# Optimization experiments

Measured on AMD Instinct MI355X. Metric: run time of the kernel, lower is better.

Reference implementation:

```python
import jax, jax.numpy as jnp
import numpy as np

N = 100000
E = 600000
D = 128


def setup_inputs() -> dict:
    key = jax.random.key(0)
    k_h, k_src, k_dst, k_W, k_b, k_H = jax.random.split(key, 6)
    h = jax.random.normal(k_h, (N, D), dtype=jnp.float32)
    src = jax.random.randint(k_src, (E,), 0, N, dtype=jnp.int64)
    dst = jax.random.randint(k_dst, (E,), 0, N, dtype=jnp.int64)
    # Linear layer params (PyTorch convention: y = x @ W_w.T + W_b)
    bound_lin = 1.0 / np.sqrt(D)
    W_w = jax.random.uniform(k_W, (D, D), dtype=jnp.float32, minval=-bound_lin, maxval=bound_lin)
    W_b = jax.random.uniform(k_b, (D,), dtype=jnp.float32, minval=-bound_lin, maxval=bound_lin)
    # H = normal(0, 1/D) + I
    H = jax.random.normal(k_H, (D, D), dtype=jnp.float32) * (1.0 / D) + jnp.eye(D, dtype=jnp.float32)
    return {"h": h, "src": src, "dst": dst, "W_w": W_w, "W_b": W_b, "H": H}


def reference(h, src, dst, W_w, W_b, H):
    # node transform: hp = W(h)
    hp = h @ W_w.T + W_b  # [N, D]
    # precompute hp @ H at node level (equivalent to (hp[dst]) @ H, cheaper)
    hpH = hp @ H  # [N, D]
    diff = hp[src] - hpH[dst]  # [E, D] edge-wise gather + sub
    score = jnp.sum(diff * diff, axis=-1)  # [E]
    return score
```

## Files before the change

kernel.cpp:

```cpp
#include <hip/hip_runtime.h>
#include <hip/hip_bf16.h>


#define D 128
#define BN 256
#define BM 64

typedef __attribute__((ext_vector_type(8))) short bf16x8;
typedef __attribute__((ext_vector_type(4))) float f32x4;

static __device__ inline unsigned short f2bf(float x) {
  union { float f; unsigned int u; } v;
  v.f = x;
  unsigned int r = v.u + 0x7fffu + ((v.u >> 16) & 1u);
  return (unsigned short)(r >> 16);
}

__global__ __launch_bounds__(256) void prep_frag_kernel(
    const float* __restrict__ Ww, const float* __restrict__ Wb,
    const float* __restrict__ H, short* __restrict__ Wfrag,
    float* __restrict__ bias_cat) {
  const int b = blockIdx.x;
  const int w = b >> 2;
  const int jt = b & 3;
  const int tid = threadIdx.x;
  const int ks = tid >> 6;
  const int lane = tid & 63;
  const int j = w * 64 + jt * 16 + (lane & 15);
  const int kb = ks * 32 + ((lane >> 4) << 3);

  unsigned short u[8];
  if (w < 2) {
    const float4 lo = *(const float4*)(Ww + j * D + kb);
    const float4 hi = *(const float4*)(Ww + j * D + kb + 4);
    u[0] = f2bf(lo.x); u[1] = f2bf(lo.y); u[2] = f2bf(lo.z); u[3] = f2bf(lo.w);
    u[4] = f2bf(hi.x); u[5] = f2bf(hi.y); u[6] = f2bf(hi.z); u[7] = f2bf(hi.w);
  } else {
    const int jj = j - D;
    float a0 = 0.f, a1 = 0.f, a2 = 0.f, a3 = 0.f;
    float a4 = 0.f, a5 = 0.f, a6 = 0.f, a7 = 0.f;
#pragma unroll 8
    for (int m = 0; m < D; ++m) {
      const float hm = H[m * D + jj];
      const float4 lo = *(const float4*)(Ww + m * D + kb);
      const float4 hi = *(const float4*)(Ww + m * D + kb + 4);
      a0 = fmaf(lo.x, hm, a0); a1 = fmaf(lo.y, hm, a1);
      a2 = fmaf(lo.z, hm, a2); a3 = fmaf(lo.w, hm, a3);
      a4 = fmaf(hi.x, hm, a4); a5 = fmaf(hi.y, hm, a5);
      a6 = fmaf(hi.z, hm, a6); a7 = fmaf(hi.w, hm, a7);
    }
    u[0] = f2bf(a0); u[1] = f2bf(a1); u[2] = f2bf(a2); u[3] = f2bf(a3);
    u[4] = f2bf(a4); u[5] = f2bf(a5); u[6] = f2bf(a6); u[7] = f2bf(a7);
  }
  const int F = ((w * 4 + jt) * 4 + ks) * 64 + lane;
  *(uint4*)(Wfrag + (size_t)F * 8) = *(const uint4*)u;

  if (tid < 16) {
    const int jb = w * 64 + jt * 16 + tid;
    float bv;
    if (w < 2) {
      bv = Wb[jb];
    } else {
      bv = 0.f;
      const int jj = jb - D;
#pragma unroll 8
      for (int m = 0; m < D; ++m) bv = fmaf(Wb[m], H[m * D + jj], bv);
    }
    bias_cat[jb] = bv;
  }
}

__global__ __launch_bounds__(256, 4) void phase1_mfma(
    const float* __restrict__ h, const short* __restrict__ Wfrag,
    const float* __restrict__ bias_cat, short* __restrict__ hp,
    short* __restrict__ hpH, int n_nodes) {
  const int tid = threadIdx.x;
  const int lane = tid & 63;
  const int w = tid >> 6;
  const int base = blockIdx.x * BM;

  f32x4 acc[4][4];
#pragma unroll
  for (int jt = 0; jt < 4; ++jt) {
    const float4 b4 =
        *(const float4*)(bias_cat + w * 64 + jt * 16 + ((lane >> 4) << 2));
    const f32x4 bi = {b4.x, b4.y, b4.z, b4.w};
#pragma unroll
    for (int nt = 0; nt < 4; ++nt) acc[jt][nt] = bi;
  }

  const bf16x8* Wf = (const bf16x8*)Wfrag;
  const int kb = (lane >> 4) << 3;

#pragma unroll
  for (int ks = 0; ks < 4; ++ks) {
    bf16x8 hf[4];
#pragma unroll
    for (int nt = 0; nt < 4; ++nt) {
      int node = base + nt * 16 + (lane & 15);
      if (node >= n_nodes) node = n_nodes - 1;
      const float* hrow = h + (size_t)node * D + ks * 32 + kb;
      const float4 lo = *(const float4*)hrow;
      const float4 hi = *(const float4*)(hrow + 4);
      union { bf16x8 v; unsigned short u[8]; } pk;
      pk.u[0] = f2bf(lo.x); pk.u[1] = f2bf(lo.y);
      pk.u[2] = f2bf(lo.z); pk.u[3] = f2bf(lo.w);
      pk.u[4] = f2bf(hi.x); pk.u[5] = f2bf(hi.y);
      pk.u[6] = f2bf(hi.z); pk.u[7] = f2bf(hi.w);
      hf[nt] = pk.v;
    }
#pragma unroll
    for (int jt = 0; jt < 4; ++jt) {
      const bf16x8 wf = Wf[(((w * 4 + jt) * 4 + ks) << 6) + lane];
#pragma unroll
      for (int nt = 0; nt < 4; ++nt) {
        acc[jt][nt] = __builtin_amdgcn_mfma_f32_16x16x32_bf16(
            wf, hf[nt], acc[jt][nt], 0, 0, 0);
      }
    }
  }

  short* outb = (w < 2) ? hp : hpH;
  const int jb = (w & 1) * 64 + ((lane >> 4) << 2);
#pragma unroll
  for (int jt = 0; jt < 4; ++jt) {
#pragma unroll
    for (int nt = 0; nt < 4; ++nt) {
      const int node = base + nt * 16 + (lane & 15);
      if (node < n_nodes) {
        uint2 pk;
        pk.x = (unsigned int)f2bf(acc[jt][nt][0]) |
               ((unsigned int)f2bf(acc[jt][nt][1]) << 16);
        pk.y = (unsigned int)f2bf(acc[jt][nt][2]) |
               ((unsigned int)f2bf(acc[jt][nt][3]) << 16);
        *(uint2*)(outb + (size_t)node * D + jb + jt * 16) = pk;
      }
    }
  }
}

__global__ __launch_bounds__(256) void edge_kernel(
    const short* __restrict__ hp, const short* __restrict__ hpH,
    const int* __restrict__ src, const int* __restrict__ dst,
    float* __restrict__ score, int n_edges) {
  const int lane = threadIdx.x & 15;
  const int e = (blockIdx.x * 256 + threadIdx.x) >> 4;
  if (e >= n_edges) return;

  const int s = src[e];
  const int d = dst[e];
  const uint4 av = *(const uint4*)(hp + (size_t)s * D + lane * 8);
  const uint4 bv = *(const uint4*)(hpH + (size_t)d * D + lane * 8);

  const unsigned int au[4] = {av.x, av.y, av.z, av.w};
  const unsigned int bu[4] = {bv.x, bv.y, bv.z, bv.w};
  float acc = 0.f;
#pragma unroll
  for (int i = 0; i < 4; ++i) {
    const float alo = __uint_as_float(au[i] << 16);
    const float ahi = __uint_as_float(au[i] & 0xffff0000u);
    const float blo = __uint_as_float(bu[i] << 16);
    const float bhi = __uint_as_float(bu[i] & 0xffff0000u);
    float t = alo - blo;
    acc = fmaf(t, t, acc);
    t = ahi - bhi;
    acc = fmaf(t, t, acc);
  }

  acc += __shfl_xor(acc, 1, 64);
  acc += __shfl_xor(acc, 2, 64);
  acc += __shfl_xor(acc, 4, 64);
  acc += __shfl_xor(acc, 8, 64);

  if (lane == 0) __builtin_nontemporal_store(acc, &score[e]);
}

extern "C" void kernel_launch(void* const* d_in, const int* in_sizes, int n_in,
                              void* d_out, int out_size, void* d_ws,
                              size_t ws_size, hipStream_t stream) {
  const float* h = (const float*)d_in[0];
  const int* src = (const int*)d_in[1];
  const int* dst = (const int*)d_in[2];
  const float* Ww = (const float*)d_in[3];
  const float* Wb = (const float*)d_in[4];
  const float* H = (const float*)d_in[5];
  float* score = (float*)d_out;

  const int n_nodes = in_sizes[0] / D;
  const int n_edges = in_sizes[1];

  char* ws = (char*)d_ws;
  short* hp = (short*)ws;
  short* hpH = hp + (size_t)n_nodes * D;
  short* Wfrag = hpH + (size_t)n_nodes * D;
  float* bias_cat = (float*)(Wfrag + 4096 * 8);

  prep_frag_kernel<<<dim3(16), dim3(256), 0, stream>>>(Ww, Wb, H, Wfrag,
                                                       bias_cat);

  const int nblk = (n_nodes + BM - 1) / BM;
  phase1_mfma<<<dim3(nblk), dim3(256), 0, stream>>>(h, Wfrag, bias_cat, hp,
                                                    hpH, n_nodes);

  const int eblk = (n_edges * 16 + 255) / 256;
  edge_kernel<<<dim3(eblk), dim3(256), 0, stream>>>(hp, hpH, src, dst, score,
                                                    n_edges);
}
```

Before: 188.2 us.

## Stage bf16 node tile in LDS once per block, shared across warps

Previously each of the 4 waves loaded and converted the same 64-node fp32 h tile from global memory, so the block read and converted it four times. Now the block cooperatively loads it once, converts it to bf16 MFMA fragments in shared memory, and every wave reads fragments from LDS after a barrier. The loops are reordered so W fragments are loaded per jt, and the occupancy hint rises from 4 to 6 blocks per CU. This adds 16KB of LDS per block and a sync, which may limit occupancy.

```diff
diff --git a/kernel.cpp b/kernel.cpp
--- a/kernel.cpp
+++ b/kernel.cpp
@@ -70,15 +70,34 @@
   }
 }
 
-__global__ __launch_bounds__(256, 4) void phase1_mfma(
+__global__ __launch_bounds__(256, 6) void phase1_mfma(
     const float* __restrict__ h, const short* __restrict__ Wfrag,
     const float* __restrict__ bias_cat, short* __restrict__ hp,
     short* __restrict__ hpH, int n_nodes) {
+  __shared__ short Hf[1024 * 8];
+
   const int tid = threadIdx.x;
   const int lane = tid & 63;
   const int w = tid >> 6;
   const int base = blockIdx.x * BM;
 
+#pragma unroll
+  for (int i = 0; i < 4; ++i) {
+    const int f = tid + i * 256;
+    const int fl = f & 63;
+    const int nt = (f >> 6) & 3;
+    const int ks = f >> 8;
+    int node = base + nt * 16 + (fl & 15);
+    if (node >= n_nodes) node = n_nodes - 1;
+    const int kb = ks * 32 + ((fl >> 4) << 3);
+    const float4 lo = *(const float4*)(h + (size_t)node * D + kb);
+    const float4 hi = *(const float4*)(h + (size_t)node * D + kb + 4);
+    unsigned short u[8];
+    u[0] = f2bf(lo.x); u[1] = f2bf(lo.y); u[2] = f2bf(lo.z); u[3] = f2bf(lo.w);
+    u[4] = f2bf(hi.x); u[5] = f2bf(hi.y); u[6] = f2bf(hi.z); u[7] = f2bf(hi.w);
+    ((uint4*)Hf)[f] = *(const uint4*)u;
+  }
+
   f32x4 acc[4][4];
 #pragma unroll
   for (int jt = 0; jt < 4; ++jt) {
@@ -89,33 +108,23 @@
     for (int nt = 0; nt < 4; ++nt) acc[jt][nt] = bi;
   }
 
+  __syncthreads();
+
   const bf16x8* Wf = (const bf16x8*)Wfrag;
-  const int kb = (lane >> 4) << 3;
-
-#pragma unroll
-  for (int ks = 0; ks < 4; ++ks) {
-    bf16x8 hf[4];
+  const bf16x8* Hf8 = (const bf16x8*)Hf;
+#pragma unroll
+  for (int jt = 0; jt < 4; ++jt) {
+    bf16x8 wf[4];
+#pragma unroll
+    for (int ks = 0; ks < 4; ++ks)
+      wf[ks] = Wf[(((w * 4 + jt) * 4 + ks) << 6) + lane];
 #pragma unroll
     for (int nt = 0; nt < 4; ++nt) {
-      int node = base + nt * 16 + (lane & 15);
-      if (node >= n_nodes) node = n_nodes - 1;
-      const float* hrow = h + (size_t)node * D + ks * 32 + kb;
-      const float4 lo = *(const float4*)hrow;
-      const float4 hi = *(const float4*)(hrow + 4);
-      union { bf16x8 v; unsigned short u[8]; } pk;
-      pk.u[0] = f2bf(lo.x); pk.u[1] = f2bf(lo.y);
-      pk.u[2] = f2bf(lo.z); pk.u[3] = f2bf(lo.w);
-      pk.u[4] = f2bf(hi.x); pk.u[5] = f2bf(hi.y);
-      pk.u[6] = f2bf(hi.z); pk.u[7] = f2bf(hi.w);
-      hf[nt] = pk.v;
-    }
-#pragma unroll
-    for (int jt = 0; jt < 4; ++jt) {
-      const bf16x8 wf = Wf[(((w * 4 + jt) * 4 + ks) << 6) + lane];
-#pragma unroll
-      for (int nt = 0; nt < 4; ++nt) {
+#pragma unroll
+      for (int ks = 0; ks < 4; ++ks) {
+        const bf16x8 hf = Hf8[((ks << 2) + nt) * 64 + lane];
         acc[jt][nt] = __builtin_amdgcn_mfma_f32_16x16x32_bf16(
-            wf, hf[nt], acc[jt][nt], 0, 0, 0);
+            wf[ks], hf, acc[jt][nt], 0, 0, 0);
       }
     }
   }
```

Result: slower. 218.0 us (+15.9%).
